# Performance work log

Hardware: AMD Instinct MI355X
Metric: run time of the kernel (lower is better)

## Reference

```python
import jax, jax.numpy as jnp
import numpy as np

H = 2048      # hidden_size
NH = 16       # num_heads
HD = H // NH  # attention_head_size = 128
NEG_BIAS = -10000.0


def setup_inputs() -> dict:
    key = jax.random.key(0)
    k1, k2, k3, k4, k5 = jax.random.split(key, 5)
    B, S = 2, 2048
    hidden_states = jax.random.normal(k1, (B, S, H), dtype=jnp.float32)
    scale = 1.0 / np.sqrt(H)
    w_qkv = jax.random.normal(k2, (H, 3 * H), dtype=jnp.float32) * scale
    b_qkv = jax.random.normal(k3, (3 * H,), dtype=jnp.float32) * 0.01
    w_out = jax.random.normal(k4, (H, H), dtype=jnp.float32) * scale
    b_out = jax.random.normal(k5, (H,), dtype=jnp.float32) * 0.01
    return {"hidden_states": hidden_states, "w_qkv": w_qkv, "b_qkv": b_qkv,
            "w_out": w_out, "b_out": b_out}


def reference(hidden_states, w_qkv, b_qkv, w_out, b_out):
    B, S, _ = hidden_states.shape
    # fused QKV projection -> [B, S, 3H]
    qkv = hidden_states @ w_qkv + b_qkv
    # split heads with 3*head_dim per head, then chunk (matches torch code)
    qkv = qkv.reshape(B, S, NH, 3 * HD).transpose(0, 2, 1, 3)  # [B, NH, S, 3*HD]
    q, k, v = jnp.split(qkv, 3, axis=-1)                       # each [B, NH, S, HD]
    # scaled scores [B, NH, S, S]
    scores = jnp.einsum('bhqd,bhkd->bhqk', q, k) / np.sqrt(HD)
    causal = jnp.tril(jnp.ones((S, S), dtype=bool))
    scores = jnp.where(causal[None, None], scores, jnp.float32(NEG_BIAS))
    probs = jax.nn.softmax(scores, axis=-1)
    ctx = jnp.einsum('bhqk,bhkd->bhqd', probs, v)  # [B, NH, S, HD]
    ctx = ctx.transpose(0, 2, 1, 3).reshape(B, S, H)
    return ctx @ w_out + b_out
```

## Files before the change

kernel.cpp:

```cpp
#include <hip/hip_runtime.h>
#include <hip/hip_bf16.h>

typedef __bf16 bf16x8 __attribute__((ext_vector_type(8)));
typedef float  f32x4  __attribute__((ext_vector_type(4)));

constexpr int   Bb   = 2;
constexpr int   Slen = 2048;
constexpr int   Hdim = 2048;
constexpr int   NHn  = 16;
constexpr int   HDd  = 128;
constexpr float QSCALE = 0.08838834764831845f;
constexpr float NEG    = -1e30f;

__device__ __forceinline__ void gld16(const __bf16* g, __bf16* l) {
    __builtin_amdgcn_global_load_lds(
        (__attribute__((address_space(1))) void*)(uintptr_t)(const void*)g,
        (__attribute__((address_space(3))) void*)l, 16, 0, 0);
}

__global__ __launch_bounds__(256) void cvt_bf16(const float* __restrict__ in,
                                                __bf16* __restrict__ out) {
    const size_t i = (size_t)(blockIdx.x * 256 + threadIdx.x) * 8;
    f32x4 a = *(const f32x4*)(in + i), b = *(const f32x4*)(in + i + 4);
    bf16x8 r;
    r[0] = (__bf16)a[0]; r[1] = (__bf16)a[1]; r[2] = (__bf16)a[2]; r[3] = (__bf16)a[3];
    r[4] = (__bf16)b[0]; r[5] = (__bf16)b[1]; r[6] = (__bf16)b[2]; r[7] = (__bf16)b[3];
    *(bf16x8*)(out + i) = r;
}

__global__ __launch_bounds__(256) void transpose_cvt(const float* __restrict__ in,
                                                     __bf16* __restrict__ out,
                                                     int R, int C) {
    __shared__ float t[64][65];
    const int c0 = blockIdx.x * 64, r0 = blockIdx.y * 64;
    const int tx = threadIdx.x & 63, ty = threadIdx.x >> 6;
#pragma unroll
    for (int i = 0; i < 16; ++i) {
        int r = i * 4 + ty;
        t[r][tx] = in[(size_t)(r0 + r) * C + c0 + tx];
    }
    __syncthreads();
#pragma unroll
    for (int i = 0; i < 16; ++i) {
        int r = i * 4 + ty;
        out[(size_t)(c0 + r) * R + r0 + tx] = (__bf16)t[tx][r];
    }
}


#define BAR    __builtin_amdgcn_s_barrier()
#define LGKM0  asm volatile("s_waitcnt lgkmcnt(0)" ::: "memory")
#define VMC(n) asm volatile("s_waitcnt vmcnt(" #n ")" ::: "memory")
#define SCHED0 __builtin_amdgcn_sched_barrier(0)

#define STAGE(op, half, tt)                                                          \
  do {                                                                               \
    const int tt_ = (tt);                                                            \
    if (tt_ < NT) {                                                                  \
      __bf16* dst_ = lds + ((tt_ & 1) << 15) + ((op) << 14) + ((half) << 13);        \
      const __bf16* src_ = (op) ? Bt : A;                                            \
      const int rb_ = (op) ? n0 : m0;                                               \
      const int k0_ = tt_ << 6;                                                      \
      _Pragma("unroll")                                                              \
      for (int i_ = 0; i_ < 2; ++i_) {                                               \
        const int c_  = (i_ << 9) + tid;                                             \
        const int rl_ = c_ >> 3;                                                     \
        const int grow_ = rb_ + ((op) ? (((rl_ >> 5) << 6) + ((half) << 5) + (rl_ & 31)) \
                                      : (((rl_ >> 6) << 7) + ((half) << 6) + (rl_ & 63))); \
        const int gk_ = k0_ + (((c_ & 7) ^ (rl_ & 7)) << 3);                         \
        gld16(src_ + (size_t)grow_ * Kdim + gk_, dst_ + (c_ << 3));                  \
      }                                                                              \
    }                                                                                \
  } while (0)

#define LDA(bufv, mh)                                                                \
  do {                                                                               \
    const __bf16* Ab_ = lds + ((bufv) << 15) + ((mh) << 13) + (wg << 12) + (l16 << 6); \
    _Pragma("unroll")                                                                \
    for (int q_ = 0; q_ < 4; ++q_)                                                   \
      _Pragma("unroll")                                                              \
      for (int kk_ = 0; kk_ < 2; ++kk_)                                              \
        af[q_][kk_] = *(const bf16x8*)(Ab_ + (q_ << 10) +                            \
                        ((((kk_ << 2) + quad) ^ (l16 & 7)) << 3));                   \
  } while (0)

#define LDB(bufv, nh)                                                                \
  do {                                                                               \
    const __bf16* Bb_ = lds + ((bufv) << 15) + 16384 + ((nh) << 13) + (gn << 11) + (l16 << 6); \
    _Pragma("unroll")                                                                \
    for (int q_ = 0; q_ < 2; ++q_)                                                   \
      _Pragma("unroll")                                                              \
      for (int kk_ = 0; kk_ < 2; ++kk_)                                              \
        bfr[((nh) << 1) + q_][kk_] = *(const bf16x8*)(Bb_ + (q_ << 10) +             \
                        ((((kk_ << 2) + quad) ^ (l16 & 7)) << 3));                   \
  } while (0)

#define MM(mh, nh)                                                                   \
  do {                                                                               \
    _Pragma("unroll")                                                                \
    for (int q_ = 0; q_ < 4; ++q_)                                                   \
      _Pragma("unroll")                                                              \
      for (int n_ = 0; n_ < 2; ++n_)                                                 \
        _Pragma("unroll")                                                            \
        for (int kk_ = 0; kk_ < 2; ++kk_)                                            \
          acc[((mh) << 2) + q_][((nh) << 1) + n_] =                                  \
            __builtin_amdgcn_mfma_f32_16x16x32_bf16(                                 \
              af[q_][kk_], bfr[((nh) << 1) + n_][kk_],                               \
              acc[((mh) << 2) + q_][((nh) << 1) + n_], 0, 0, 0);                     \
  } while (0)

__global__ __launch_bounds__(512, 2) void gemm8(
    const __bf16* __restrict__ A, const __bf16* __restrict__ Bt,
    const float* __restrict__ bias, int Kdim, int Ndim,
    __bf16* __restrict__ Qo, __bf16* __restrict__ Ko, __bf16* __restrict__ Vto) {
    __shared__ __bf16 lds[65536];
    const int tid  = threadIdx.x;
    const int lane = tid & 63, wave = tid >> 6;
    const int quad = lane >> 4, l16 = lane & 15;
    const int wg = wave >> 2;
    const int gn = wave & 3;
    const int m0 = blockIdx.y * 256, n0 = blockIdx.x * 256;
    const int NT = Kdim >> 6;

    f32x4  acc[8][4] = {};
    bf16x8 af[4][2];
    bf16x8 bfr[4][2];

    STAGE(0, 0, 0); STAGE(1, 0, 0); STAGE(1, 1, 0); STAGE(0, 1, 0);
    STAGE(0, 0, 1); STAGE(1, 0, 1); STAGE(1, 1, 1);
    VMC(6);
    BAR;

    for (int t = 0; t < NT; ++t) {
        const int cb = t & 1;
        LDA(cb, 0); LDB(cb, 0);
        STAGE(0, 1, t + 1);
        BAR; LGKM0;
        __builtin_amdgcn_s_setprio(1); MM(0, 0); __builtin_amdgcn_s_setprio(0);
        BAR;
        LDB(cb, 1);
        STAGE(0, 0, t + 2);
        BAR; LGKM0;
        __builtin_amdgcn_s_setprio(1); MM(0, 1); __builtin_amdgcn_s_setprio(0);
        BAR;
        LDA(cb, 1);
        STAGE(1, 0, t + 2);
        BAR; LGKM0;
        __builtin_amdgcn_s_setprio(1); MM(1, 1); __builtin_amdgcn_s_setprio(0);
        BAR;
        STAGE(1, 1, t + 2);
        if (t < NT - 2) { VMC(6); } else { VMC(0); }
        BAR;
        __builtin_amdgcn_s_setprio(1); MM(1, 0); __builtin_amdgcn_s_setprio(0);
        BAR;
    }

#pragma unroll
    for (int mi = 0; mi < 8; ++mi) {
#pragma unroll
        for (int r = 0; r < 4; ++r) {
            const int m = m0 + wg * 128 + (mi >> 2) * 64 + (mi & 3) * 16 + quad * 4 + r;
            const int b = m >> 11, s = m & 2047;
#pragma unroll
            for (int ni = 0; ni < 4; ++ni) {
                const int cc = n0 + gn * 64 + (ni >> 1) * 32 + (ni & 1) * 16 + l16;
                float val = acc[mi][ni][r] + bias[cc];
                const int h = cc / 384;
                const int rr = cc - h * 384;
                const size_t hb = ((size_t)(b * NHn + h) * Slen + s);
                if (rr < 128)
                    Qo[hb * HDd + rr] = (__bf16)(val * QSCALE);
                else if (rr < 256)
                    Ko[hb * HDd + (rr - 128)] = (__bf16)val;
                else
                    Vto[((size_t)(b * NHn + h) * HDd + (rr - 256)) * Slen + s] = (__bf16)val;
            }
        }
    }
}


#define STA1(half, tt)                                                               \
  do {                                                                               \
    const int tt_ = (tt);                                                            \
    if (tt_ < NT) {                                                                  \
      __bf16* dst_ = lds2 + ((tt_ & 1) ? 24576 : 0) + ((half) << 12);                \
      const int k0_ = tt_ << 6;                                                      \
      const int c_  = tid;                                 \
      const int rl_ = c_ >> 3;                           \
      const int grow_ = m0 + ((rl_ >> 5) << 6) + ((half) << 5) + (rl_ & 31);         \
      const int gk_ = k0_ + (((c_ & 7) ^ (rl_ & 7)) << 3);                           \
      gld16(A + (size_t)grow_ * Kdim + gk_, dst_ + (c_ << 3));                       \
    }                                                                                \
  } while (0)

#define STB1(half, tt)                                                               \
  do {                                                                               \
    const int tt_ = (tt);                                                            \
    if (tt_ < NT) {                                                                  \
      __bf16* dst_ = lds2 + ((tt_ & 1) ? 24576 : 0) + 8192 + ((half) << 13);         \
      const int k0_ = tt_ << 6;                                                      \
      _Pragma("unroll")                                                              \
      for (int i_ = 0; i_ < 2; ++i_) {                                               \
        const int c_  = (i_ << 9) + tid;                                \
        const int rl_ = c_ >> 3;                        \
        const int grow_ = n0 + ((rl_ >> 5) << 6) + ((half) << 5) + (rl_ & 31);       \
        const int gk_ = k0_ + (((c_ & 7) ^ (rl_ & 7)) << 3);                         \
        gld16(Bt + (size_t)grow_ * Kdim + gk_, dst_ + (c_ << 3));                    \
      }                                                                              \
    }                                                                                \
  } while (0)

#define LDA1(bufv, h)                                                                \
  do {                                                                               \
    const __bf16* Ab_ = lds2 + ((bufv) ? 24576 : 0) + ((h) << 12) + (wg << 11) + (l16 << 6); \
    _Pragma("unroll")                                                                \
    for (int q_ = 0; q_ < 2; ++q_)                                                   \
      _Pragma("unroll")                                                              \
      for (int kk_ = 0; kk_ < 2; ++kk_)                                              \
        af1[q_][kk_] = *(const bf16x8*)(Ab_ + (q_ << 10) +                           \
                        ((((kk_ << 2) + quad) ^ (l16 & 7)) << 3));                   \
  } while (0)

#define LDB1(bufv, nh)                                                               \
  do {                                                                               \
    const __bf16* Bb_ = lds2 + ((bufv) ? 24576 : 0) + 8192 + ((nh) << 13) + (gn << 11) + (l16 << 6); \
    _Pragma("unroll")                                                                \
    for (int q_ = 0; q_ < 2; ++q_)                                                   \
      _Pragma("unroll")                                                              \
      for (int kk_ = 0; kk_ < 2; ++kk_)                                              \
        bfr1[((nh) << 1) + q_][kk_] = *(const bf16x8*)(Bb_ + (q_ << 10) +            \
                        ((((kk_ << 2) + quad) ^ (l16 & 7)) << 3));                   \
  } while (0)

#define MM1(h, nh)                                                                   \
  do {                                                                               \
    _Pragma("unroll")                                                                \
    for (int q_ = 0; q_ < 2; ++q_)                                                   \
      _Pragma("unroll")                                                              \
      for (int n_ = 0; n_ < 2; ++n_)                                                 \
        _Pragma("unroll")                                                            \
        for (int kk_ = 0; kk_ < 2; ++kk_)                                            \
          acc1[((h) << 1) + q_][((nh) << 1) + n_] =                                  \
            __builtin_amdgcn_mfma_f32_16x16x32_bf16(                                 \
              af1[q_][kk_], bfr1[((nh) << 1) + n_][kk_],                             \
              acc1[((h) << 1) + q_][((nh) << 1) + n_], 0, 0, 0);                     \
  } while (0)

__global__ __launch_bounds__(512, 2) void gemm_bm128(
    const __bf16* __restrict__ A, const __bf16* __restrict__ Bt,
    const float* __restrict__ bias, int Kdim, int Ndim,
    float* __restrict__ Cout) {
    __shared__ __bf16 lds2[49152];
    const int tid  = threadIdx.x;
    const int lane = tid & 63, wave = tid >> 6;
    const int quad = lane >> 4, l16 = lane & 15;
    const int wg = wave >> 2;
    const int gn = wave & 3;
    const int m0 = blockIdx.y * 128, n0 = blockIdx.x * 256;
    const int NT = Kdim >> 6;

    f32x4  acc1[4][4] = {};
    bf16x8 af1[2][2];
    bf16x8 bfr1[4][2];

    STA1(0, 0); STB1(0, 0); STB1(1, 0); STA1(1, 0);
    STA1(0, 1); STB1(0, 1); STB1(1, 1);
    SCHED0;
    VMC(5);
    BAR;

    for (int t = 0; t < NT; ++t) {
        const int cb = t & 1;
        LDA1(cb, 0); LDB1(cb, 0);
        STA1(1, t + 1);
        SCHED0;
        BAR; LGKM0; SCHED0;
        __builtin_amdgcn_s_setprio(1); MM1(0, 0); __builtin_amdgcn_s_setprio(0);
        BAR;
        LDB1(cb, 1);
        STA1(0, t + 2);
        SCHED0;
        BAR; LGKM0; SCHED0;
        __builtin_amdgcn_s_setprio(1); MM1(0, 1); __builtin_amdgcn_s_setprio(0);
        BAR;
        LDA1(cb, 1);
        STB1(0, t + 2);
        SCHED0;
        BAR; LGKM0; SCHED0;
        __builtin_amdgcn_s_setprio(1); MM1(1, 1); __builtin_amdgcn_s_setprio(0);
        BAR;
        STB1(1, t + 2);
        SCHED0;
        if (t < NT - 2) { VMC(5); } else { VMC(0); }
        BAR;
        __builtin_amdgcn_s_setprio(1); MM1(1, 0); __builtin_amdgcn_s_setprio(0);
        BAR;
    }

#pragma unroll
    for (int mi = 0; mi < 4; ++mi) {
#pragma unroll
        for (int r = 0; r < 4; ++r) {
            const int m = m0 + wg * 64 + (mi >> 1) * 32 + (mi & 1) * 16 + quad * 4 + r;
#pragma unroll
            for (int ni = 0; ni < 4; ++ni) {
                const int cc = n0 + gn * 64 + (ni >> 1) * 32 + (ni & 1) * 16 + l16;
                Cout[(size_t)m * Ndim + cc] = acc1[mi][ni][r] + bias[cc];
            }
        }
    }
}


#define ASTAGE(tt)                                                                   \
  do {                                                                               \
    const int tt_ = (tt);                                                            \
    if (tt_ < ktiles) {                                                              \
      const int kb_ = tt_ << 6;                                                      \
      __bf16* kd_ = Ks + ((tt_ & 1) << 13);                                          \
      __bf16* vd_ = Vs + ((tt_ & 1) << 13);                                          \
      _Pragma("unroll")                                                              \
      for (int i_ = 0; i_ < 2; ++i_) {                                               \
        const int c_ = (i_ << 9) + tid;                        \
        const int kr_ = c_ >> 4, kc_ = c_ & 15;           \
        gld16(Kb + (size_t)(kb_ + kr_) * HDd + ((kc_ ^ (kr_ & 7)) << 3),             \
              kd_ + (c_ << 3));                                                      \
        const int vr_ = c_ >> 3, vc_ = c_ & 7;               \
        gld16(Vb + (size_t)vr_ * Slen + kb_ + ((vc_ ^ (vr_ & 7)) << 3),              \
              vd_ + (c_ << 3));                                                      \
      }                                                                              \
    }                                                                                \
  } while (0)

__global__ __launch_bounds__(512, 4) void attn_k(const __bf16* __restrict__ Q,
                                                 const __bf16* __restrict__ Kmat,
                                                 const __bf16* __restrict__ Vt,
                                                 __bf16* __restrict__ ctx) {
    __shared__ __bf16 Ks[2 * 64 * 128];
    __shared__ __bf16 Vs[2 * 128 * 64];
    __shared__ __bf16 Ps[8 * 16 * 64];
    const int tid = threadIdx.x, lane = tid & 63, wave = tid >> 6;
    const int quad = lane >> 4, l16 = lane & 15;

    const int flat = blockIdx.x + (blockIdx.y << 4);
    const int x    = flat & 7;
    const int k    = flat >> 3;
    const int u    = (k >> 1) & 15;
    const int s_   = (k ^ (k >> 5)) & 1;
    const int qt   = s_ ? (15 - u) : u;
    const int bh   = x * 4 + (k & 1) + ((k >> 5) << 1);
    const int b = bh >> 4, h = bh & 15;
    const __bf16* Qb = Q    + (size_t)bh * Slen * HDd;
    const __bf16* Kb = Kmat + (size_t)bh * Slen * HDd;
    const __bf16* Vb = Vt   + (size_t)bh * HDd * Slen;
    const int q0 = qt * 128;
    const int qa = q0 + wave * 16 + l16;
    const int qc = q0 + wave * 16 + quad * 4;
    const int swz = (l16 & 7);

    bf16x8 qf[4];
#pragma unroll
    for (int kk = 0; kk < 4; ++kk)
        qf[kk] = *(const bf16x8*)(Qb + (size_t)qa * HDd + kk * 32 + quad * 8);

    f32x4 accO[8] = {};
    float m_i[4] = {NEG, NEG, NEG, NEG};
    float l_i[4] = {0.f, 0.f, 0.f, 0.f};
    __bf16* Pw = Ps + wave * 1024;

    const int ktiles = 2 * qt + 2;

    ASTAGE(0);
    for (int kt = 0; kt < ktiles; ++kt) {
        const int cur = kt & 1;
        const int kb0 = kt * 64;
        ASTAGE(kt + 1);
        SCHED0;
        if (kt + 1 < ktiles) { VMC(4); } else { VMC(0); }
        BAR;

        const __bf16* Kt = Ks + (cur << 13);
        const __bf16* Vc = Vs + (cur << 13);

        f32x4 sc[4];
        __builtin_amdgcn_s_setprio(1);
#pragma unroll
        for (int nk = 0; nk < 4; ++nk) {
            f32x4 z = {0.f, 0.f, 0.f, 0.f};
#pragma unroll
            for (int kk = 0; kk < 4; ++kk) {
                bf16x8 kf = *(const bf16x8*)(Kt + (nk * 16 + l16) * 128 +
                                             (((kk << 2) + quad) ^ swz) * 8);
                z = __builtin_amdgcn_mfma_f32_16x16x32_bf16(qf[kk], kf, z, 0, 0, 0);
            }
            sc[nk] = z;
        }
        __builtin_amdgcn_s_setprio(0);
        if (kt >= ktiles - 2) {
#pragma unroll
            for (int nk = 0; nk < 4; ++nk) {
                const int kg = kb0 + nk * 16 + l16;
#pragma unroll
                for (int r = 0; r < 4; ++r)
                    if (kg > qc + r) sc[nk][r] = NEG;
            }
        }
#pragma unroll
        for (int r = 0; r < 4; ++r) {
            float mm = fmaxf(fmaxf(sc[0][r], sc[1][r]), fmaxf(sc[2][r], sc[3][r]));
            mm = fmaxf(mm, __shfl_xor(mm, 1));
            mm = fmaxf(mm, __shfl_xor(mm, 2));
            mm = fmaxf(mm, __shfl_xor(mm, 4));
            mm = fmaxf(mm, __shfl_xor(mm, 8));
            const float mnew = fmaxf(m_i[r], mm);
            const float alpha = __expf(m_i[r] - mnew);
            float ls = 0.f;
#pragma unroll
            for (int nk = 0; nk < 4; ++nk) {
                float p = __expf(sc[nk][r] - mnew);
                sc[nk][r] = p;
                ls += p;
            }
            ls += __shfl_xor(ls, 1);
            ls += __shfl_xor(ls, 2);
            ls += __shfl_xor(ls, 4);
            ls += __shfl_xor(ls, 8);
            l_i[r] = l_i[r] * alpha + ls;
            m_i[r] = mnew;
#pragma unroll
            for (int nd = 0; nd < 8; ++nd) accO[nd][r] *= alpha;
        }

#pragma unroll
        for (int nk = 0; nk < 4; ++nk)
#pragma unroll
            for (int r = 0; r < 4; ++r) {
                const int row = quad * 4 + r, col = nk * 16 + l16;
                Pw[row * 64 + (((col >> 3) ^ (row & 7)) << 3) + (col & 7)] =
                    (__bf16)sc[nk][r];
            }
        bf16x8 pf[2];
#pragma unroll
        for (int kk = 0; kk < 2; ++kk)
            pf[kk] = *(const bf16x8*)(Pw + l16 * 64 + ((((kk << 2) + quad) ^ swz) << 3));

        __builtin_amdgcn_s_setprio(1);
#pragma unroll
        for (int nd = 0; nd < 8; ++nd)
#pragma unroll
            for (int kk = 0; kk < 2; ++kk) {
                bf16x8 vf = *(const bf16x8*)(Vc + (nd * 16 + l16) * 64 +
                                             ((((kk << 2) + quad) ^ swz) << 3));
                accO[nd] = __builtin_amdgcn_mfma_f32_16x16x32_bf16(pf[kk], vf, accO[nd], 0, 0, 0);
            }
        __builtin_amdgcn_s_setprio(0);
        LGKM0; SCHED0;
        BAR;
    }

#pragma unroll
    for (int nd = 0; nd < 8; ++nd)
#pragma unroll
        for (int r = 0; r < 4; ++r) {
            const int s = q0 + wave * 16 + quad * 4 + r;
            const int d = nd * 16 + l16;
            const float o = accO[nd][r] / fmaxf(l_i[r], 1e-20f);
            ctx[((size_t)b * Slen + s) * Hdim + h * HDd + d] = (__bf16)o;
        }
}

extern "C" void kernel_launch(void* const* d_in, const int* in_sizes, int n_in,
                              void* d_out, int out_size, void* d_ws, size_t ws_size,
                              hipStream_t stream) {
    const float* hs   = (const float*)d_in[0];
    const float* wqkv = (const float*)d_in[1];
    const float* bqkv = (const float*)d_in[2];
    const float* wout = (const float*)d_in[3];
    const float* bout = (const float*)d_in[4];
    float* out = (float*)d_out;

    __bf16* ws    = (__bf16*)d_ws;
    __bf16* wqkvT = ws;
    __bf16* woutT = wqkvT + (size_t)6144 * 2048;
    __bf16* Qs    = woutT + (size_t)2048 * 2048;
    __bf16* Kms   = Qs  + (size_t)Bb * NHn * Slen * HDd;
    __bf16* Vts   = Kms + (size_t)Bb * NHn * Slen * HDd;
    __bf16* ctx   = Vts + (size_t)Bb * NHn * Slen * HDd;
    __bf16* hsb   = ctx;

    cvt_bf16<<<(Bb * Slen * Hdim) / (256 * 8), 256, 0, stream>>>(hs, hsb);
    transpose_cvt<<<dim3(6144 / 64, 2048 / 64), 256, 0, stream>>>(wqkv, wqkvT, 2048, 6144);
    transpose_cvt<<<dim3(2048 / 64, 2048 / 64), 256, 0, stream>>>(wout, woutT, 2048, 2048);
    gemm8<<<dim3(6144 / 256, 4096 / 256), 512, 0, stream>>>(
        hsb, wqkvT, bqkv, Hdim, 3 * Hdim, Qs, Kms, Vts);
    attn_k<<<dim3(Slen / 128, Bb * NHn), 512, 0, stream>>>(Qs, Kms, Vts, ctx);
    gemm_bm128<<<dim3(2048 / 256, 4096 / 128), 512, 0, stream>>>(
        ctx, woutT, bout, Hdim, Hdim, out);
}
```

Before: 420.7 us.

## Software-pipeline LDS fragment loads with MFMA in QKV GEMM using double A registers

Restructures the QKV projection GEMM main loop so LDS-to-register fragment loads for the next quarter-tile (and the next K-tile's first A/B fragments) are issued before the current MFMA block, using two A-fragment register sets. The loop drops from eight barriers to three per K iteration, and the vmcnt waits are retuned to match the new order of global-to-LDS stages. This aims to hide LDS read latency behind matrix-core work and cut barrier stalls, at the cost of more VGPRs and occupancy risk under launch_bounds(512,2). The output GEMM also loses its SCHED0 scheduling barriers, letting the compiler reorder freely.

Result: no change. 419.7 us (-0.3%).

```diff
diff --git a/kernel.cpp b/kernel.cpp
--- a/kernel.cpp
+++ b/kernel.cpp
@@ -73,29 +73,29 @@
     }                                                                                \
   } while (0)
 
-#define LDA(bufv, mh)                                                                \
+#define LDA_(bufv, mh, DST)                                                          \
   do {                                                                               \
     const __bf16* Ab_ = lds + ((bufv) << 15) + ((mh) << 13) + (wg << 12) + (l16 << 6); \
     _Pragma("unroll")                                                                \
     for (int q_ = 0; q_ < 4; ++q_)                                                   \
       _Pragma("unroll")                                                              \
       for (int kk_ = 0; kk_ < 2; ++kk_)                                              \
-        af[q_][kk_] = *(const bf16x8*)(Ab_ + (q_ << 10) +                            \
+        DST[q_][kk_] = *(const bf16x8*)(Ab_ + (q_ << 10) +                           \
                         ((((kk_ << 2) + quad) ^ (l16 & 7)) << 3));                   \
   } while (0)
 
-#define LDB(bufv, nh)                                                                \
+#define LDB_(bufv, nh, base)                                                         \
   do {                                                                               \
     const __bf16* Bb_ = lds + ((bufv) << 15) + 16384 + ((nh) << 13) + (gn << 11) + (l16 << 6); \
     _Pragma("unroll")                                                                \
     for (int q_ = 0; q_ < 2; ++q_)                                                   \
       _Pragma("unroll")                                                              \
       for (int kk_ = 0; kk_ < 2; ++kk_)                                              \
-        bfr[((nh) << 1) + q_][kk_] = *(const bf16x8*)(Bb_ + (q_ << 10) +             \
+        bfr[(base) + q_][kk_] = *(const bf16x8*)(Bb_ + (q_ << 10) +                  \
                         ((((kk_ << 2) + quad) ^ (l16 & 7)) << 3));                   \
   } while (0)
 
-#define MM(mh, nh)                                                                   \
+#define MMX(AF, mh, nb)                                                              \
   do {                                                                               \
     _Pragma("unroll")                                                                \
     for (int q_ = 0; q_ < 4; ++q_)                                                   \
@@ -103,10 +103,33 @@
       for (int n_ = 0; n_ < 2; ++n_)                                                 \
         _Pragma("unroll")                                                            \
         for (int kk_ = 0; kk_ < 2; ++kk_)                                            \
-          acc[((mh) << 2) + q_][((nh) << 1) + n_] =                                  \
+          acc[((mh) << 2) + q_][(nb) + n_] =                                         \
             __builtin_amdgcn_mfma_f32_16x16x32_bf16(                                 \
-              af[q_][kk_], bfr[((nh) << 1) + n_][kk_],                               \
-              acc[((mh) << 2) + q_][((nh) << 1) + n_], 0, 0, 0);                     \
+              AF[q_][kk_], bfr[(nb) + n_][kk_],                                      \
+              acc[((mh) << 2) + q_][(nb) + n_], 0, 0, 0);                            \
+  } while (0)
+
+#define GTILE(t, cb)                                                                 \
+  do {                                                                               \
+    LGKM0;                      \
+    __builtin_amdgcn_s_setprio(1); MMX(af_a, 0, 0); __builtin_amdgcn_s_setprio(0);   \
+    LDB_((cb), 1, 2);                \
+    STAGE(0, 1, (t) + 1);          \
+    BAR;                                                                             \
+    LGKM0;                                                          \
+    __builtin_amdgcn_s_setprio(1); MMX(af_a, 0, 2); __builtin_amdgcn_s_setprio(0);   \
+    LDA_((cb), 1, af_b);                                         \
+    STAGE(0, 0, (t) + 2);           \
+    STAGE(1, 0, (t) + 2);                          \
+    BAR;                                                                             \
+    LGKM0;                                                           \
+    __builtin_amdgcn_s_setprio(1); MMX(af_b, 1, 0); __builtin_amdgcn_s_setprio(0);   \
+    STAGE(1, 1, (t) + 2);           \
+    if ((t) < NT - 2) { VMC(8); } else { VMC(0); }        \
+    BAR;                                                                             \
+    if ((t) + 1 < NT) { LDA_((cb) ^ 1, 0, af_a); LDB_((cb) ^ 1, 0, 0); }             \
+    __builtin_amdgcn_s_setprio(1); MMX(af_b, 1, 2); __builtin_amdgcn_s_setprio(0);   \
+    if ((t) < NT - 2) { VMC(6); } else { VMC(0); }               \
   } while (0)
 
 __global__ __launch_bounds__(512, 2) void gemm8(
@@ -123,36 +146,18 @@
     const int NT = Kdim >> 6;
 
     f32x4  acc[8][4] = {};
-    bf16x8 af[4][2];
+    bf16x8 af_a[4][2];
+    bf16x8 af_b[4][2];
     bf16x8 bfr[4][2];
 
     STAGE(0, 0, 0); STAGE(1, 0, 0); STAGE(1, 1, 0); STAGE(0, 1, 0);
     STAGE(0, 0, 1); STAGE(1, 0, 1); STAGE(1, 1, 1);
     VMC(6);
     BAR;
+    LDA_(0, 0, af_a); LDB_(0, 0, 0);
 
     for (int t = 0; t < NT; ++t) {
-        const int cb = t & 1;
-        LDA(cb, 0); LDB(cb, 0);
-        STAGE(0, 1, t + 1);
-        BAR; LGKM0;
-        __builtin_amdgcn_s_setprio(1); MM(0, 0); __builtin_amdgcn_s_setprio(0);
-        BAR;
-        LDB(cb, 1);
-        STAGE(0, 0, t + 2);
-        BAR; LGKM0;
-        __builtin_amdgcn_s_setprio(1); MM(0, 1); __builtin_amdgcn_s_setprio(0);
-        BAR;
-        LDA(cb, 1);
-        STAGE(1, 0, t + 2);
-        BAR; LGKM0;
-        __builtin_amdgcn_s_setprio(1); MM(1, 1); __builtin_amdgcn_s_setprio(0);
-        BAR;
-        STAGE(1, 1, t + 2);
-        if (t < NT - 2) { VMC(6); } else { VMC(0); }
-        BAR;
-        __builtin_amdgcn_s_setprio(1); MM(1, 0); __builtin_amdgcn_s_setprio(0);
-        BAR;
+        GTILE(t, (t & 1));
     }
 
 #pragma unroll
@@ -266,7 +271,6 @@
 
     STA1(0, 0); STB1(0, 0); STB1(1, 0); STA1(1, 0);
     STA1(0, 1); STB1(0, 1); STB1(1, 1);
-    SCHED0;
     VMC(5);
     BAR;
 
@@ -274,24 +278,20 @@
         const int cb = t & 1;
         LDA1(cb, 0); LDB1(cb, 0);
         STA1(1, t + 1);
-        SCHED0;
-        BAR; LGKM0; SCHED0;
+        BAR; LGKM0;
         __builtin_amdgcn_s_setprio(1); MM1(0, 0); __builtin_amdgcn_s_setprio(0);
         BAR;
         LDB1(cb, 1);
         STA1(0, t + 2);
-        SCHED0;
-        BAR; LGKM0; SCHED0;
+        BAR; LGKM0;
         __builtin_amdgcn_s_setprio(1); MM1(0, 1); __builtin_amdgcn_s_setprio(0);
         BAR;
         LDA1(cb, 1);
         STB1(0, t + 2);
-        SCHED0;
-        BAR; LGKM0; SCHED0;
+        BAR; LGKM0;
         __builtin_amdgcn_s_setprio(1); MM1(1, 1); __builtin_amdgcn_s_setprio(0);
         BAR;
         STB1(1, t + 2);
-        SCHED0;
         if (t < NT - 2) { VMC(5); } else { VMC(0); }
         BAR;
         __builtin_amdgcn_s_setprio(1); MM1(1, 0); __builtin_amdgcn_s_setprio(0);
```
